# Kernel tuning notes

Hardware: AMD Instinct MI355X
Metric: run time of the kernel (lower is better)

The kernel has to match this reference:

```python
import jax, jax.numpy as jnp
import numpy as np

N_NODES = 50000
N_EDGES = 800000
DIM_IN = 128
DIM_OUT = 64


def setup_inputs() -> dict:
    key = jax.random.key(0)
    k1, k2, k3, k4 = jax.random.split(key, 4)
    x = jax.random.normal(k1, (N_NODES, DIM_IN), dtype=jnp.float32)
    edge_index = jax.random.randint(k2, (2, N_EDGES), 0, N_NODES, dtype=jnp.int64)
    W = jax.random.normal(k3, (DIM_IN, DIM_OUT), dtype=jnp.float32) / np.sqrt(DIM_IN)
    b = jax.random.normal(k4, (DIM_OUT,), dtype=jnp.float32) * 0.01
    return {"x": x, "edge_index": edge_index, "W": W, "b": b}


def reference(x, edge_index, W, b):
    # Faithful PyG GCNConv: add self-loops, symmetric deg normalization,
    # linear transform then normalized scatter-add aggregation, then bias.
    N = x.shape[0]
    h = x @ W  # [N, dim_out] — transform before propagate (PyG order)

    loops = jnp.arange(N, dtype=edge_index.dtype)
    src = jnp.concatenate([edge_index[0], loops])  # [E+N]
    dst = jnp.concatenate([edge_index[1], loops])  # [E+N]

    ones = jnp.ones(src.shape[0], dtype=h.dtype)
    deg = jax.ops.segment_sum(ones, dst, num_segments=N)  # in-degree incl. self-loop
    dinv = jnp.where(deg > 0, jax.lax.rsqrt(deg), 0.0)
    norm = dinv[src] * dinv[dst]  # [E+N]

    msgs = h[src] * norm[:, None]  # gather + scale
    out = jax.ops.segment_sum(msgs, dst, num_segments=N) + b  # scatter-add
    return jax.nn.log_softmax(out, axis=1)
```

## Files before the change

kernel.cpp:

```cpp
#include <hip/hip_runtime.h>
#include <hip/hip_fp16.h>
#include <cstdint>
#include <cstddef>

#define N_NODES 50000
#define N_EDGES 800000
#define DIM_IN  128
#define DIM_OUT 64

#define B2SHIFT 8
#define B2NODES 256
#define NB2     ((N_NODES + B2NODES - 1) / B2NODES)
#define EB      4096
#define SORTB   ((N_EDGES + EB - 1) / EB)
#define NE4     (N_EDGES / 4)
#define CAPB    4864
#define GROWS   128
#define GEMMB   ((N_NODES + GROWS - 1) / GROWS)
#define GPAD    16
#define NEGRP   ((N_NODES + 31) / 32)

typedef _Float16 f16x8 __attribute__((ext_vector_type(8)));
typedef float    f32x4 __attribute__((ext_vector_type(4)));

__global__ __launch_bounds__(256) void k_zero(int* __restrict__ gcnt) {
    const int i = blockIdx.x * 256 + threadIdx.x;
    if (i < NB2 * GPAD) gcnt[i] = 0;
}

__global__ __launch_bounds__(256) void kFG(const int* __restrict__ ei,
                                           int* __restrict__ gcnt,
                                           unsigned* __restrict__ pairs,
                                           const float* __restrict__ x,
                                           const float* __restrict__ W,
                                           __half* __restrict__ h) {
    const int t = threadIdx.x;
    if (blockIdx.x < SORTB) {
        __shared__ int hcnt[B2NODES];
        __shared__ int cur[B2NODES];
        const int blk = blockIdx.x;
        hcnt[t] = 0;
        __syncthreads();
        const int4* src4 = (const int4*)ei;
        const int4* dst4 = (const int4*)(ei + N_EDGES);
        const int g0 = blk * (EB / 4);
#pragma unroll
        for (int it = 0; it < EB / 1024; ++it) {
            const int g = g0 + it * 256 + t;
            if (g < NE4) {
                const int4 d = dst4[g];
                atomicAdd(&hcnt[d.x >> B2SHIFT], 1);
                atomicAdd(&hcnt[d.y >> B2SHIFT], 1);
                atomicAdd(&hcnt[d.z >> B2SHIFT], 1);
                atomicAdd(&hcnt[d.w >> B2SHIFT], 1);
            }
        }
        __syncthreads();
        {
            const int c = hcnt[t];
            const int base = c ? atomicAdd(&gcnt[t * GPAD], c) : 0;
            cur[t] = t * CAPB + base;
        }
        __syncthreads();
#pragma unroll
        for (int it = 0; it < EB / 1024; ++it) {
            const int g = g0 + it * 256 + t;
            if (g < NE4) {
                const int4 sv = src4[g];
                const int4 dv = dst4[g];
                int b, p;
                b = dv.x >> B2SHIFT; p = atomicAdd(&cur[b], 1);
                if (p < b * CAPB + CAPB) pairs[p] = ((unsigned)sv.x << 16) | (unsigned)dv.x;
                b = dv.y >> B2SHIFT; p = atomicAdd(&cur[b], 1);
                if (p < b * CAPB + CAPB) pairs[p] = ((unsigned)sv.y << 16) | (unsigned)dv.y;
                b = dv.z >> B2SHIFT; p = atomicAdd(&cur[b], 1);
                if (p < b * CAPB + CAPB) pairs[p] = ((unsigned)sv.z << 16) | (unsigned)dv.z;
                b = dv.w >> B2SHIFT; p = atomicAdd(&cur[b], 1);
                if (p < b * CAPB + CAPB) pairs[p] = ((unsigned)sv.w << 16) | (unsigned)dv.w;
            }
        }
    } else {
        const int u = blockIdx.x - SORTB;
        const int w = t >> 6;
        const int l = t & 63;
        const int q = l >> 4;
        const int m16 = l & 15;

        f16x8 bf[4][4];
#pragma unroll
        for (int kc = 0; kc < 4; ++kc)
#pragma unroll
            for (int ct = 0; ct < 4; ++ct) {
                const float* wp = W + (size_t)(kc * 32 + q * 8) * DIM_OUT + ct * 16 + m16;
                f16x8 v;
#pragma unroll
                for (int j = 0; j < 8; ++j) v[j] = (_Float16)wp[(size_t)j * DIM_OUT];
                bf[kc][ct] = v;
            }

        const int base = u * GROWS + w * 32;
#pragma unroll
        for (int rt = 0; rt < 2; ++rt) {
            const int m0 = base + rt * 16;
            int mrow = m0 + m16;
            if (mrow >= N_NODES) mrow = N_NODES - 1;

            f16x8 af[4];
#pragma unroll
            for (int kc = 0; kc < 4; ++kc) {
                const float4* xp = (const float4*)(x + (size_t)mrow * DIM_IN + kc * 32 + q * 8);
                const float4 p0 = xp[0], p1 = xp[1];
                f16x8 a;
                a[0] = (_Float16)p0.x; a[1] = (_Float16)p0.y;
                a[2] = (_Float16)p0.z; a[3] = (_Float16)p0.w;
                a[4] = (_Float16)p1.x; a[5] = (_Float16)p1.y;
                a[6] = (_Float16)p1.z; a[7] = (_Float16)p1.w;
                af[kc] = a;
            }

            f32x4 acc[4];
#pragma unroll
            for (int ct = 0; ct < 4; ++ct) acc[ct] = (f32x4){0.f, 0.f, 0.f, 0.f};
#pragma unroll
            for (int kc = 0; kc < 4; ++kc)
#pragma unroll
                for (int ct = 0; ct < 4; ++ct)
                    acc[ct] = __builtin_amdgcn_mfma_f32_16x16x32_f16(af[kc], bf[kc][ct], acc[ct], 0, 0, 0);

#pragma unroll
            for (int reg = 0; reg < 4; ++reg) {
                const int r = m0 + q * 4 + reg;
                if (r < N_NODES) {
#pragma unroll
                    for (int ct = 0; ct < 4; ++ct)
                        h[(size_t)r * DIM_OUT + ct * 16 + m16] = __float2half(acc[ct][reg]);
                }
            }
        }
    }
}

__global__ __launch_bounds__(512) void kSort(const unsigned* __restrict__ pairs,
                                             const int* __restrict__ gcnt,
                                             unsigned short* __restrict__ csr,
                                             int2* __restrict__ nodeoff2,
                                             __half* __restrict__ h) {
    __shared__ int cnt[B2NODES];
    __shared__ int cur[B2NODES];
    __shared__ float sdinv[B2NODES];
    __shared__ int wsum[4];
    __shared__ unsigned short lcsr[CAPB];
    const int b = blockIdx.x, t = threadIdx.x;
    const int eb = b * CAPB;
    const int count = min(gcnt[b * GPAD], CAPB);
    const int ee = eb + count;

    if (t < B2NODES) cnt[t] = 0;
    __syncthreads();

    {
        int i = eb + t;
        for (; i + 1536 < ee; i += 2048) {
            const unsigned p0 = pairs[i];
            const unsigned p1 = pairs[i + 512];
            const unsigned p2 = pairs[i + 1024];
            const unsigned p3 = pairs[i + 1536];
            atomicAdd(&cnt[p0 & (B2NODES - 1)], 1);
            atomicAdd(&cnt[p1 & (B2NODES - 1)], 1);
            atomicAdd(&cnt[p2 & (B2NODES - 1)], 1);
            atomicAdd(&cnt[p3 & (B2NODES - 1)], 1);
        }
        for (; i < ee; i += 512) atomicAdd(&cnt[pairs[i] & (B2NODES - 1)], 1);
    }
    __syncthreads();

    if (t < B2NODES) {
        const int lane = t & 63;
        const int v = cnt[t];
        int xs = v;
#pragma unroll
        for (int off = 1; off < 64; off <<= 1) {
            int y = __shfl_up(xs, off);
            if (lane >= off) xs += y;
        }
        cur[t] = xs;
        if (lane == 63) wsum[t >> 6] = xs;
    }
    __syncthreads();
    if (t == 0) {
        int acc = 0;
#pragma unroll
        for (int w2 = 0; w2 < 4; ++w2) { const int v2 = wsum[w2]; wsum[w2] = acc; acc += v2; }
    }
    __syncthreads();
    if (t < B2NODES) {
        const int v = cnt[t];
        const int excl = cur[t] - v + wsum[t >> 6];
        sdinv[t] = rsqrtf((float)(v + 1));
        const int n = (b << B2SHIFT) + t;
        if (n < N_NODES) nodeoff2[n] = make_int2(eb + excl, v);
        cur[t] = excl;
    }
    __syncthreads();

    for (int i = eb + t; i < ee; i += 512) {
        const unsigned p = pairs[i];
        const int q = atomicAdd(&cur[p & (B2NODES - 1)], 1);
        lcsr[q] = (unsigned short)(p >> 16);
    }
    __syncthreads();

    {
        const int cw = (count + 1) >> 1;
        const unsigned* l32 = (const unsigned*)lcsr;
        unsigned* c32 = (unsigned*)(csr + eb);
        for (int i2 = t; i2 < cw; i2 += 512) c32[i2] = l32[i2];
    }
    {
        f16x8* h8w = (f16x8*)h;
        for (int idx = t; idx < B2NODES * 8; idx += 512) {
            const int r = idx >> 3;
            const int n = (b << B2SHIFT) + r;
            if (n < N_NODES) {
                const float d = sdinv[r];
                f16x8 v = h8w[(size_t)n * 8 + (idx & 7)];
#pragma unroll
                for (int j = 0; j < 8; ++j) v[j] = (_Float16)((float)v[j] * d);
                h8w[(size_t)n * 8 + (idx & 7)] = v;
            }
        }
    }
}

__global__ __launch_bounds__(256) void kE_agg(const int2* __restrict__ nodeoff2,
                                              const unsigned short* __restrict__ csr,
                                              const __half* __restrict__ h,
                                              const float* __restrict__ bvec,
                                              float* __restrict__ out) {
    const int t = threadIdx.x;
    const int ew = t >> 3, sl = t & 7;
    const int n = blockIdx.x * 32 + ew;
    if (n >= N_NODES) return;
    const f16x8* __restrict__ h8 = (const f16x8*)h;

    const int2 off = nodeoff2[n];
    const int s0 = off.x, s1 = off.x + off.y;

    const f16x8 hv = h8[(size_t)n * 8 + sl];
    float a[8];
#pragma unroll
    for (int j = 0; j < 8; ++j) a[j] = (float)hv[j];

    int i = s0;
    for (; i + 4 <= s1; i += 4) {
        const int c0 = csr[i + 0];
        const int c1 = csr[i + 1];
        const int c2 = csr[i + 2];
        const int c3 = csr[i + 3];
        const f16x8 v0 = h8[(size_t)c0 * 8 + sl];
        const f16x8 v1 = h8[(size_t)c1 * 8 + sl];
        const f16x8 v2 = h8[(size_t)c2 * 8 + sl];
        const f16x8 v3 = h8[(size_t)c3 * 8 + sl];
#pragma unroll
        for (int j = 0; j < 8; ++j)
            a[j] += (float)v0[j] + (float)v1[j] + (float)v2[j] + (float)v3[j];
    }
    for (; i < s1; ++i) {
        const f16x8 v0 = h8[(size_t)csr[i] * 8 + sl];
#pragma unroll
        for (int j = 0; j < 8; ++j) a[j] += (float)v0[j];
    }

    const float4 b0 = *(const float4*)&bvec[8 * sl];
    const float4 b1 = *(const float4*)&bvec[8 * sl + 4];
    const float di = rsqrtf((float)(off.y + 1));
    float v[8];
    v[0] = a[0] * di + b0.x; v[1] = a[1] * di + b0.y;
    v[2] = a[2] * di + b0.z; v[3] = a[3] * di + b0.w;
    v[4] = a[4] * di + b1.x; v[5] = a[5] * di + b1.y;
    v[6] = a[6] * di + b1.z; v[7] = a[7] * di + b1.w;

    float m = v[0];
#pragma unroll
    for (int j = 1; j < 8; ++j) m = fmaxf(m, v[j]);
#pragma unroll
    for (int o = 4; o > 0; o >>= 1) m = fmaxf(m, __shfl_xor(m, o));
    float s = 0.f;
#pragma unroll
    for (int j = 0; j < 8; ++j) s += __expf(v[j] - m);
#pragma unroll
    for (int o = 4; o > 0; o >>= 1) s += __shfl_xor(s, o);
    const float ls = m + __logf(s);

    float4 o0, o1;
    o0.x = v[0] - ls; o0.y = v[1] - ls; o0.z = v[2] - ls; o0.w = v[3] - ls;
    o1.x = v[4] - ls; o1.y = v[5] - ls; o1.z = v[6] - ls; o1.w = v[7] - ls;
    *(float4*)&out[(size_t)n * DIM_OUT + 8 * sl]     = o0;
    *(float4*)&out[(size_t)n * DIM_OUT + 8 * sl + 4] = o1;
}

extern "C" void kernel_launch(void* const* d_in, const int* in_sizes, int n_in,
                              void* d_out, int out_size, void* d_ws, size_t ws_size,
                              hipStream_t stream) {
    const float* x  = (const float*)d_in[0];
    const int*   ei = (const int*)d_in[1];
    const float* W  = (const float*)d_in[2];
    const float* b  = (const float*)d_in[3];
    float* out = (float*)d_out;

    char* ws = (char*)d_ws;
    __half*         h        = (__half*)ws;         ws += (size_t)N_NODES * DIM_OUT * sizeof(__half);
    unsigned*       pairs    = (unsigned*)ws;       ws += (size_t)NB2 * CAPB * sizeof(unsigned);
    unsigned short* csr      = (unsigned short*)ws; ws += (size_t)NB2 * CAPB * sizeof(unsigned short);
    int2*           nodeoff2 = (int2*)ws;           ws += (size_t)N_NODES * sizeof(int2);
    int*            gcnt     = (int*)ws;            ws += (size_t)NB2 * GPAD * sizeof(int);

    k_zero <<<(NB2 * GPAD + 255) / 256, 256, 0, stream>>>(gcnt);
    kFG    <<<SORTB + GEMMB, 256, 0, stream>>>(ei, gcnt, pairs, x, W, h);
    kSort  <<<NB2, 512, 0, stream>>>(pairs, gcnt, csr, nodeoff2, h);
    kE_agg <<<NEGRP, 256, 0, stream>>>(nodeoff2, csr, h, b, out);
}
```

Baseline: 114.2 us.

## Replace global-atomic bucket scatter with fixed-size per-block runs and drop zero kernel

After: 121.0 us. +5.9%, slower.

```diff
diff --git a/kernel.cpp b/kernel.cpp
--- a/kernel.cpp
+++ b/kernel.cpp
@@ -14,71 +14,52 @@
 #define EB      4096
 #define SORTB   ((N_EDGES + EB - 1) / EB)
 #define NE4     (N_EDGES / 4)
+#define RUNSZ   64
+#define RUNTOT  (SORTB * RUNSZ)
 #define CAPB    4864
 #define GROWS   128
 #define GEMMB   ((N_NODES + GROWS - 1) / GROWS)
-#define GPAD    16
+#define HSTRIDE 256
 #define NEGRP   ((N_NODES + 31) / 32)
 
 typedef _Float16 f16x8 __attribute__((ext_vector_type(8)));
 typedef float    f32x4 __attribute__((ext_vector_type(4)));
 
-__global__ __launch_bounds__(256) void k_zero(int* __restrict__ gcnt) {
-    const int i = blockIdx.x * 256 + threadIdx.x;
-    if (i < NB2 * GPAD) gcnt[i] = 0;
-}
-
 __global__ __launch_bounds__(256) void kFG(const int* __restrict__ ei,
-                                           int* __restrict__ gcnt,
+                                           int* __restrict__ hist,
                                            unsigned* __restrict__ pairs,
                                            const float* __restrict__ x,
                                            const float* __restrict__ W,
                                            __half* __restrict__ h) {
     const int t = threadIdx.x;
     if (blockIdx.x < SORTB) {
-        __shared__ int hcnt[B2NODES];
-        __shared__ int cur[B2NODES];
+        __shared__ int curb[B2NODES];
         const int blk = blockIdx.x;
-        hcnt[t] = 0;
+        curb[t] = 0;
         __syncthreads();
         const int4* src4 = (const int4*)ei;
         const int4* dst4 = (const int4*)(ei + N_EDGES);
         const int g0 = blk * (EB / 4);
+        const int rbase = blk * RUNSZ;
 #pragma unroll
         for (int it = 0; it < EB / 1024; ++it) {
             const int g = g0 + it * 256 + t;
             if (g < NE4) {
-                const int4 d = dst4[g];
-                atomicAdd(&hcnt[d.x >> B2SHIFT], 1);
-                atomicAdd(&hcnt[d.y >> B2SHIFT], 1);
-                atomicAdd(&hcnt[d.z >> B2SHIFT], 1);
-                atomicAdd(&hcnt[d.w >> B2SHIFT], 1);
+                const int4 dv = dst4[g];
+                const int4 sv = src4[g];
+                int b, p;
+                b = dv.x >> B2SHIFT; p = atomicAdd(&curb[b], 1);
+                if (p < RUNSZ) pairs[(size_t)b * RUNTOT + rbase + p] = ((unsigned)sv.x << 16) | (unsigned)dv.x;
+                b = dv.y >> B2SHIFT; p = atomicAdd(&curb[b], 1);
+                if (p < RUNSZ) pairs[(size_t)b * RUNTOT + rbase + p] = ((unsigned)sv.y << 16) | (unsigned)dv.y;
+                b = dv.z >> B2SHIFT; p = atomicAdd(&curb[b], 1);
+                if (p < RUNSZ) pairs[(size_t)b * RUNTOT + rbase + p] = ((unsigned)sv.z << 16) | (unsigned)dv.z;
+                b = dv.w >> B2SHIFT; p = atomicAdd(&curb[b], 1);
+                if (p < RUNSZ) pairs[(size_t)b * RUNTOT + rbase + p] = ((unsigned)sv.w << 16) | (unsigned)dv.w;
             }
         }
         __syncthreads();
-        {
-            const int c = hcnt[t];
-            const int base = c ? atomicAdd(&gcnt[t * GPAD], c) : 0;
-            cur[t] = t * CAPB + base;
-        }
-        __syncthreads();
-#pragma unroll
-        for (int it = 0; it < EB / 1024; ++it) {
-            const int g = g0 + it * 256 + t;
-            if (g < NE4) {
-                const int4 sv = src4[g];
-                const int4 dv = dst4[g];
-                int b, p;
-                b = dv.x >> B2SHIFT; p = atomicAdd(&cur[b], 1);
-                if (p < b * CAPB + CAPB) pairs[p] = ((unsigned)sv.x << 16) | (unsigned)dv.x;
-                b = dv.y >> B2SHIFT; p = atomicAdd(&cur[b], 1);
-                if (p < b * CAPB + CAPB) pairs[p] = ((unsigned)sv.y << 16) | (unsigned)dv.y;
-                b = dv.z >> B2SHIFT; p = atomicAdd(&cur[b], 1);
-                if (p < b * CAPB + CAPB) pairs[p] = ((unsigned)sv.z << 16) | (unsigned)dv.z;
-                b = dv.w >> B2SHIFT; p = atomicAdd(&cur[b], 1);
-                if (p < b * CAPB + CAPB) pairs[p] = ((unsigned)sv.w << 16) | (unsigned)dv.w;
-            }
-        }
+        hist[blk * HSTRIDE + t] = min(curb[t], RUNSZ);
     } else {
         const int u = blockIdx.x - SORTB;
         const int w = t >> 6;
@@ -141,7 +122,7 @@
 }
 
 __global__ __launch_bounds__(512) void kSort(const unsigned* __restrict__ pairs,
-                                             const int* __restrict__ gcnt,
+                                             const int* __restrict__ hist,
                                              unsigned short* __restrict__ csr,
                                              int2* __restrict__ nodeoff2,
                                              __half* __restrict__ h) {
@@ -149,28 +130,20 @@
     __shared__ int cur[B2NODES];
     __shared__ float sdinv[B2NODES];
     __shared__ int wsum[4];
+    __shared__ int tot;
+    __shared__ int hlen[SORTB];
     __shared__ unsigned short lcsr[CAPB];
     const int b = blockIdx.x, t = threadIdx.x;
     const int eb = b * CAPB;
-    const int count = min(gcnt[b * GPAD], CAPB);
-    const int ee = eb + count;
-
+    const unsigned* __restrict__ pb = pairs + (size_t)b * RUNTOT;
+
+    if (t < SORTB) hlen[t] = hist[t * HSTRIDE + b];
     if (t < B2NODES) cnt[t] = 0;
     __syncthreads();
 
-    {
-        int i = eb + t;
-        for (; i + 1536 < ee; i += 2048) {
-            const unsigned p0 = pairs[i];
-            const unsigned p1 = pairs[i + 512];
-            const unsigned p2 = pairs[i + 1024];
-            const unsigned p3 = pairs[i + 1536];
-            atomicAdd(&cnt[p0 & (B2NODES - 1)], 1);
-            atomicAdd(&cnt[p1 & (B2NODES - 1)], 1);
-            atomicAdd(&cnt[p2 & (B2NODES - 1)], 1);
-            atomicAdd(&cnt[p3 & (B2NODES - 1)], 1);
-        }
-        for (; i < ee; i += 512) atomicAdd(&cnt[pairs[i] & (B2NODES - 1)], 1);
+    for (int f = t; f < RUNTOT; f += 512) {
+        if ((f & (RUNSZ - 1)) < hlen[f >> 6])
+            atomicAdd(&cnt[pb[f] & (B2NODES - 1)], 1);
     }
     __syncthreads();
 
@@ -191,6 +164,7 @@
         int acc = 0;
 #pragma unroll
         for (int w2 = 0; w2 < 4; ++w2) { const int v2 = wsum[w2]; wsum[w2] = acc; acc += v2; }
+        tot = min(acc, CAPB);
     }
     __syncthreads();
     if (t < B2NODES) {
@@ -203,15 +177,17 @@
     }
     __syncthreads();
 
-    for (int i = eb + t; i < ee; i += 512) {
-        const unsigned p = pairs[i];
-        const int q = atomicAdd(&cur[p & (B2NODES - 1)], 1);
-        lcsr[q] = (unsigned short)(p >> 16);
+    for (int f = t; f < RUNTOT; f += 512) {
+        if ((f & (RUNSZ - 1)) < hlen[f >> 6]) {
+            const unsigned p = pb[f];
+            const int q = atomicAdd(&cur[p & (B2NODES - 1)], 1);
+            if (q < CAPB) lcsr[q] = (unsigned short)(p >> 16);
+        }
     }
     __syncthreads();
 
     {
-        const int cw = (count + 1) >> 1;
+        const int cw = (tot + 1) >> 1;
         const unsigned* l32 = (const unsigned*)lcsr;
         unsigned* c32 = (unsigned*)(csr + eb);
         for (int i2 = t; i2 < cw; i2 += 512) c32[i2] = l32[i2];
@@ -310,13 +286,12 @@
 
     char* ws = (char*)d_ws;
     __half*         h        = (__half*)ws;         ws += (size_t)N_NODES * DIM_OUT * sizeof(__half);
-    unsigned*       pairs    = (unsigned*)ws;       ws += (size_t)NB2 * CAPB * sizeof(unsigned);
+    unsigned*       pairs    = (unsigned*)ws;       ws += (size_t)NB2 * RUNTOT * sizeof(unsigned);
     unsigned short* csr      = (unsigned short*)ws; ws += (size_t)NB2 * CAPB * sizeof(unsigned short);
     int2*           nodeoff2 = (int2*)ws;           ws += (size_t)N_NODES * sizeof(int2);
-    int*            gcnt     = (int*)ws;            ws += (size_t)NB2 * GPAD * sizeof(int);
-
-    k_zero <<<(NB2 * GPAD + 255) / 256, 256, 0, stream>>>(gcnt);
-    kFG    <<<SORTB + GEMMB, 256, 0, stream>>>(ei, gcnt, pairs, x, W, h);
-    kSort  <<<NB2, 512, 0, stream>>>(pairs, gcnt, csr, nodeoff2, h);
+    int*            hist     = (int*)ws;            ws += (size_t)SORTB * HSTRIDE * sizeof(int);
+
+    kFG    <<<SORTB + GEMMB, 256, 0, stream>>>(ei, hist, pairs, x, W, h);
+    kSort  <<<NB2, 512, 0, stream>>>(pairs, hist, csr, nodeoff2, h);
     kE_agg <<<NEGRP, 256, 0, stream>>>(nodeoff2, csr, h, b, out);
 }
```

## Apply source normalization during aggregation instead of pre-scaling h in sort

Applied to the files above, without the earlier changes.

Result: slower. 117.1 us (+2.5%).

```diff
diff --git a/kernel.cpp b/kernel.cpp
--- a/kernel.cpp
+++ b/kernel.cpp
@@ -22,11 +22,6 @@
 
 typedef _Float16 f16x8 __attribute__((ext_vector_type(8)));
 typedef float    f32x4 __attribute__((ext_vector_type(4)));
-
-__global__ __launch_bounds__(256) void k_zero(int* __restrict__ gcnt) {
-    const int i = blockIdx.x * 256 + threadIdx.x;
-    if (i < NB2 * GPAD) gcnt[i] = 0;
-}
 
 __global__ __launch_bounds__(256) void kFG(const int* __restrict__ ei,
                                            int* __restrict__ gcnt,
@@ -144,10 +139,9 @@
                                              const int* __restrict__ gcnt,
                                              unsigned short* __restrict__ csr,
                                              int2* __restrict__ nodeoff2,
-                                             __half* __restrict__ h) {
+                                             float* __restrict__ dinv) {
     __shared__ int cnt[B2NODES];
     __shared__ int cur[B2NODES];
-    __shared__ float sdinv[B2NODES];
     __shared__ int wsum[4];
     __shared__ unsigned short lcsr[CAPB];
     const int b = blockIdx.x, t = threadIdx.x;
@@ -196,9 +190,11 @@
     if (t < B2NODES) {
         const int v = cnt[t];
         const int excl = cur[t] - v + wsum[t >> 6];
-        sdinv[t] = rsqrtf((float)(v + 1));
         const int n = (b << B2SHIFT) + t;
-        if (n < N_NODES) nodeoff2[n] = make_int2(eb + excl, v);
+        if (n < N_NODES) {
+            nodeoff2[n] = make_int2(eb + excl, v);
+            dinv[n] = rsqrtf((float)(v + 1));
+        }
         cur[t] = excl;
     }
     __syncthreads();
@@ -216,25 +212,12 @@
         unsigned* c32 = (unsigned*)(csr + eb);
         for (int i2 = t; i2 < cw; i2 += 512) c32[i2] = l32[i2];
     }
-    {
-        f16x8* h8w = (f16x8*)h;
-        for (int idx = t; idx < B2NODES * 8; idx += 512) {
-            const int r = idx >> 3;
-            const int n = (b << B2SHIFT) + r;
-            if (n < N_NODES) {
-                const float d = sdinv[r];
-                f16x8 v = h8w[(size_t)n * 8 + (idx & 7)];
-#pragma unroll
-                for (int j = 0; j < 8; ++j) v[j] = (_Float16)((float)v[j] * d);
-                h8w[(size_t)n * 8 + (idx & 7)] = v;
-            }
-        }
-    }
 }
 
 __global__ __launch_bounds__(256) void kE_agg(const int2* __restrict__ nodeoff2,
                                               const unsigned short* __restrict__ csr,
                                               const __half* __restrict__ h,
+                                              const float* __restrict__ dinv,
                                               const float* __restrict__ bvec,
                                               float* __restrict__ out) {
     const int t = threadIdx.x;
@@ -245,35 +228,52 @@
 
     const int2 off = nodeoff2[n];
     const int s0 = off.x, s1 = off.x + off.y;
+    const float di = rsqrtf((float)(off.y + 1));
 
     const f16x8 hv = h8[(size_t)n * 8 + sl];
     float a[8];
 #pragma unroll
-    for (int j = 0; j < 8; ++j) a[j] = (float)hv[j];
+    for (int j = 0; j < 8; ++j) a[j] = (float)hv[j] * di;
 
     int i = s0;
+    for (; i + 8 <= s1; i += 8) {
+        int   c[8];
+        float d[8];
+        f16x8 v[8];
+#pragma unroll
+        for (int j = 0; j < 8; ++j) c[j] = csr[i + j];
+#pragma unroll
+        for (int j = 0; j < 8; ++j) d[j] = dinv[c[j]];
+#pragma unroll
+        for (int j = 0; j < 8; ++j) v[j] = h8[(size_t)c[j] * 8 + sl];
+#pragma unroll
+        for (int j = 0; j < 8; ++j)
+#pragma unroll
+            for (int k = 0; k < 8; ++k) a[k] += (float)v[j][k] * d[j];
+    }
     for (; i + 4 <= s1; i += 4) {
-        const int c0 = csr[i + 0];
-        const int c1 = csr[i + 1];
-        const int c2 = csr[i + 2];
-        const int c3 = csr[i + 3];
+        const int c0 = csr[i + 0], c1 = csr[i + 1];
+        const int c2 = csr[i + 2], c3 = csr[i + 3];
+        const float d0 = dinv[c0], d1 = dinv[c1], d2 = dinv[c2], d3 = dinv[c3];
         const f16x8 v0 = h8[(size_t)c0 * 8 + sl];
         const f16x8 v1 = h8[(size_t)c1 * 8 + sl];
         const f16x8 v2 = h8[(size_t)c2 * 8 + sl];
         const f16x8 v3 = h8[(size_t)c3 * 8 + sl];
 #pragma unroll
         for (int j = 0; j < 8; ++j)
-            a[j] += (float)v0[j] + (float)v1[j] + (float)v2[j] + (float)v3[j];
+            a[j] += (float)v0[j] * d0 + (float)v1[j] * d1
+                  + (float)v2[j] * d2 + (float)v3[j] * d3;
     }
     for (; i < s1; ++i) {
-        const f16x8 v0 = h8[(size_t)csr[i] * 8 + sl];
-#pragma unroll
-        for (int j = 0; j < 8; ++j) a[j] += (float)v0[j];
+        const int c = csr[i];
+        const float d = dinv[c];
+        const f16x8 v0 = h8[(size_t)c * 8 + sl];
+#pragma unroll
+        for (int j = 0; j < 8; ++j) a[j] += (float)v0[j] * d;
     }
 
     const float4 b0 = *(const float4*)&bvec[8 * sl];
     const float4 b1 = *(const float4*)&bvec[8 * sl + 4];
-    const float di = rsqrtf((float)(off.y + 1));
     float v[8];
     v[0] = a[0] * di + b0.x; v[1] = a[1] * di + b0.y;
     v[2] = a[2] * di + b0.z; v[3] = a[3] * di + b0.w;
@@ -313,10 +313,11 @@
     unsigned*       pairs    = (unsigned*)ws;       ws += (size_t)NB2 * CAPB * sizeof(unsigned);
     unsigned short* csr      = (unsigned short*)ws; ws += (size_t)NB2 * CAPB * sizeof(unsigned short);
     int2*           nodeoff2 = (int2*)ws;           ws += (size_t)N_NODES * sizeof(int2);
+    float*          dinv     = (float*)ws;          ws += (size_t)N_NODES * sizeof(float);
     int*            gcnt     = (int*)ws;            ws += (size_t)NB2 * GPAD * sizeof(int);
 
-    k_zero <<<(NB2 * GPAD + 255) / 256, 256, 0, stream>>>(gcnt);
+    hipMemsetAsync(gcnt, 0, (size_t)NB2 * GPAD * sizeof(int), stream);
     kFG    <<<SORTB + GEMMB, 256, 0, stream>>>(ei, gcnt, pairs, x, W, h);
-    kSort  <<<NB2, 512, 0, stream>>>(pairs, gcnt, csr, nodeoff2, h);
-    kE_agg <<<NEGRP, 256, 0, stream>>>(nodeoff2, csr, h, b, out);
+    kSort  <<<NB2, 512, 0, stream>>>(pairs, gcnt, csr, nodeoff2, dinv);
+    kE_agg <<<NEGRP, 256, 0, stream>>>(nodeoff2, csr, h, dinv, b, out);
 }
```
